# Optimization experiments

Measured on AMD Instinct MI355X. Metric: run time of the kernel, lower is better.

Reference implementation:

```python
import jax, jax.numpy as jnp
import numpy as np

N_START = 2
N_SUBUNITS = 1_000_000


def setup_inputs() -> dict:
    key = jax.random.key(0)
    k1, k2 = jax.random.split(key)
    # TMV-like helical parameters (Angstroms / degrees)
    rise = jnp.asarray(1.408, dtype=jnp.float32)
    twist = jnp.asarray(22.03, dtype=jnp.float32)
    initial_displacement = jax.random.normal(k1, (3,), dtype=jnp.float32) * 10.0
    # proper random rotation matrix for the first subunit via QR
    A = jax.random.normal(k2, (3, 3), dtype=jnp.float32)
    Q, _ = jnp.linalg.qr(A)
    initial_rotation = Q.astype(jnp.float32)
    return {
        "rise": rise,
        "twist": twist,
        "initial_displacement": initial_displacement,
        "initial_rotation": initial_rotation,
        "n_start": N_START,
        "n_subunits": N_SUBUNITS,
    }


def _helix_lattice(rise, twist_rad, r0, T0, n_start, n_subunits):
    """Closed-form rewrite of the affine lax.scan recurrences.

    Original position recurrence: r_{k+1} = R @ r_k + rise*ez with
    R = [[c, s, 0], [-s, c, 0], [0, 0, 1]] = Mz(-twist), so
    r_k = Mz(-k*twist) @ r0 + k*rise*ez (ez is invariant under Mz).
    Original rotation recurrence: T_k = (R^T)^k @ T0 = Mz(k*twist) @ T0.
    Symmetry rotation R_n = Mz(-sym_angle); Mz matrices commute/add angles.
    """
    dtype = r0.dtype
    k = jnp.arange(n_subunits, dtype=dtype)                                # (S,)
    sym = 2.0 * jnp.pi * jnp.arange(n_start, dtype=dtype) / n_start       # (H,)

    # ---- positions: Mz(-(sym + k*twist)) @ r0 + (k*rise - rise*S/2)*ez ----
    a = -(sym[:, None] + k[None, :] * twist_rad)                          # (H, S)
    ca, sa = jnp.cos(a), jnp.sin(a)
    x0, y0, z0 = r0[0], r0[1], r0[2]
    px = ca * x0 - sa * y0
    py = sa * x0 + ca * y0
    pz = jnp.broadcast_to(z0 + k * rise - rise * n_subunits / 2, a.shape)
    positions = jnp.stack([px, py, pz], axis=-1).reshape(n_start * n_subunits, 3)

    # ---- rotations: Mz(k*twist - sym) @ T0 ----
    b = k[None, :] * twist_rad - sym[:, None]                             # (H, S)
    cb, sb = jnp.cos(b), jnp.sin(b)
    zeros = jnp.zeros_like(cb)
    ones = jnp.ones_like(cb)
    M = jnp.stack(
        [
            jnp.stack([cb, -sb, zeros], axis=-1),
            jnp.stack([sb, cb, zeros], axis=-1),
            jnp.stack([zeros, zeros, ones], axis=-1),
        ],
        axis=-2,
    )                                                                      # (H, S, 3, 3)
    rotations = jnp.einsum("hsij,jk->hsik", M, T0).reshape(
        n_start * n_subunits, 3, 3
    )
    return positions, rotations


def reference(rise, twist, initial_displacement, initial_rotation, n_start, n_subunits):
    twist_rad = jnp.deg2rad(twist)  # degrees=True in the original module
    return _helix_lattice(
        rise, twist_rad, initial_displacement, initial_rotation, n_start, n_subunits
    )
```

## Files before the change

kernel.cpp:

```cpp
#include <hip/hip_runtime.h>
#include <math.h>

static constexpr int S_SUB   = 1000000;
static constexpr int H_START = 2;
static constexpr int CHK     = 128;
static constexpr int NCH_H   = (S_SUB + CHK - 1) / CHK;
static constexpr int NCH     = NCH_H * H_START;
static constexpr int TPB     = 256;
static constexpr int WPB     = TPB / 64;
static constexpr int NBLK    = 977;
static constexpr int NWAVE   = NBLK * WPB;

__global__ __launch_bounds__(256) void helix_kernel(
    const float* __restrict__ rise_p, const float* __restrict__ twist_p,
    const float* __restrict__ disp, const float* __restrict__ rot0,
    float* __restrict__ out )
{
    __shared__ alignas(16) float lds[WPB][CHK * 12];

    const int w = threadIdx.x >> 6;
    const int l = threadIdx.x & 63;
    float* __restrict__ PB = lds[w];
    float* __restrict__ RB = lds[w] + CHK * 3;

    const double t_rev  = (double)twist_p[0] * (1.0 / 360.0);
    const float  rise_f = rise_p[0];
    const float  zoff_f = (float)((double)disp[2]
                                  - (double)rise_p[0] * (double)S_SUB * 0.5);
    const float  x0 = disp[0], y0 = disp[1];
    const float  T00 = rot0[0], T01 = rot0[1], T02 = rot0[2];
    const float  T10 = rot0[3], T11 = rot0[4], T12 = rot0[5];
    const float  T20 = rot0[6], T21 = rot0[7], T22 = rot0[8];

    const int wave0 = blockIdx.x * WPB + w;
    for (int wid = wave0; wid < NCH; wid += NWAVE) {
        const int   h     = (wid >= NCH_H) ? 1 : 0;
        const int   c     = wid - h * NCH_H;
        const int   kbase = c * CHK;
        const int   nsub  = min(CHK, S_SUB - kbase);
        const float sgn   = h ? -1.0f : 1.0f;

#pragma unroll
        for (int j = 0; j < 2; ++j) {
            if (j * 64 < nsub) {
                const int    i   = l + 64 * j;
                const int    k   = kbase + i;
                const double trd = (double)k * t_rev;
                const float  fr  = (float)(trd - floor(trd));
                const float  c0  = sgn * __builtin_amdgcn_cosf(fr);
                const float  s0  = sgn * __builtin_amdgcn_sinf(fr);
                PB[i * 3 + 0] = c0 * x0 + s0 * y0;
                PB[i * 3 + 1] = c0 * y0 - s0 * x0;
                PB[i * 3 + 2] = (float)k * rise_f + zoff_f;
                RB[i * 9 + 0] = c0 * T00 - s0 * T10;
                RB[i * 9 + 1] = c0 * T01 - s0 * T11;
                RB[i * 9 + 2] = c0 * T02 - s0 * T12;
                RB[i * 9 + 3] = s0 * T00 + c0 * T10;
                RB[i * 9 + 4] = s0 * T01 + c0 * T11;
                RB[i * 9 + 5] = s0 * T02 + c0 * T12;
                RB[i * 9 + 6] = T20;
                RB[i * 9 + 7] = T21;
                RB[i * 9 + 8] = T22;
            }
        }

        const size_t hs = (size_t)h * S_SUB + (size_t)kbase;

        float2* __restrict__ pg = reinterpret_cast<float2*>(out + hs * 3);
        const int nf2p = (nsub * 3) >> 1;
#pragma unroll
        for (int i2 = 0; i2 < 3; ++i2) {
            const int m = l + 64 * i2;
            if (m < nf2p)
                pg[m] = *reinterpret_cast<const float2*>(&PB[2 * m]);
        }

        float2* __restrict__ rg = reinterpret_cast<float2*>(
            out + (size_t)3 * H_START * S_SUB + hs * 9);
        const int nf2r = (nsub * 9) >> 1;
#pragma unroll
        for (int i2 = 0; i2 < 9; ++i2) {
            const int m = l + 64 * i2;
            if (m < nf2r)
                rg[m] = *reinterpret_cast<const float2*>(&RB[2 * m]);
        }
    }
}

extern "C" void kernel_launch(void* const* d_in, const int* in_sizes, int n_in,
                              void* d_out, int out_size, void* d_ws, size_t ws_size,
                              hipStream_t stream) {
    const float* rise  = (const float*)d_in[0];
    const float* twist = (const float*)d_in[1];
    const float* disp  = (const float*)d_in[2];
    const float* rot0  = (const float*)d_in[3];
    float* out = (float*)d_out;

    helix_kernel<<<dim3(NBLK), TPB, 0, stream>>>(rise, twist, disp, rot0, out);
}
```

Before: 21.42 us.

## Drop LDS staging and compute each output float4 directly per thread

Replaces the per-wave LDS staging with float2 copies by a grid-stride loop in which each thread produces one float4 of the flat output. For its four elements the thread recomputes sine and cosine for up to two subunits and selects the value by index arithmetic. This removes LDS traffic and barriers and widens stores to 16 bytes. In exchange the trig and double-precision fraction work is repeated for every float4 rather than once per subunit, and the integer divides and selects add ALU work.

```diff
diff --git a/kernel.cpp b/kernel.cpp
--- a/kernel.cpp
+++ b/kernel.cpp
@@ -3,26 +3,22 @@
 
 static constexpr int S_SUB   = 1000000;
 static constexpr int H_START = 2;
-static constexpr int CHK     = 128;
-static constexpr int NCH_H   = (S_SUB + CHK - 1) / CHK;
-static constexpr int NCH     = NCH_H * H_START;
+static constexpr int POS_E   = 3 * H_START * S_SUB;
+static constexpr int TOT_E   = 12 * H_START * S_SUB;
+static constexpr int NQ      = TOT_E / 4;
 static constexpr int TPB     = 256;
-static constexpr int WPB     = TPB / 64;
-static constexpr int NBLK    = 977;
-static constexpr int NWAVE   = NBLK * WPB;
+static constexpr int NBLK    = 2048;
+static constexpr int NTHR    = NBLK * TPB;
+
+__device__ __forceinline__ float sel3(int x, float a, float b, float c) {
+    return x == 0 ? a : (x == 1 ? b : c);
+}
 
 __global__ __launch_bounds__(256) void helix_kernel(
     const float* __restrict__ rise_p, const float* __restrict__ twist_p,
     const float* __restrict__ disp, const float* __restrict__ rot0,
     float* __restrict__ out )
 {
-    __shared__ alignas(16) float lds[WPB][CHK * 12];
-
-    const int w = threadIdx.x >> 6;
-    const int l = threadIdx.x & 63;
-    float* __restrict__ PB = lds[w];
-    float* __restrict__ RB = lds[w] + CHK * 3;
-
     const double t_rev  = (double)twist_p[0] * (1.0 / 360.0);
     const float  rise_f = rise_p[0];
     const float  zoff_f = (float)((double)disp[2]
@@ -32,58 +28,80 @@
     const float  T10 = rot0[3], T11 = rot0[4], T12 = rot0[5];
     const float  T20 = rot0[6], T21 = rot0[7], T22 = rot0[8];
 
-    const int wave0 = blockIdx.x * WPB + w;
-    for (int wid = wave0; wid < NCH; wid += NWAVE) {
-        const int   h     = (wid >= NCH_H) ? 1 : 0;
-        const int   c     = wid - h * NCH_H;
-        const int   kbase = c * CHK;
-        const int   nsub  = min(CHK, S_SUB - kbase);
-        const float sgn   = h ? -1.0f : 1.0f;
+    float4* __restrict__ o4 = reinterpret_cast<float4*>(out);
+
+    for (int q = blockIdx.x * TPB + threadIdx.x; q < NQ; q += NTHR) {
+        const int e = q * 4;
+        float v0, v1, v2, v3;
+
+        if (e < POS_E) {
+            const int h  = (e >= 3 * S_SUB) ? 1 : 0;
+            const int e2 = e - h * 3 * S_SUB;
+            const int k0 = e2 / 3;
+            const int m0 = e2 - k0 * 3;
+            const float sgn = h ? -1.0f : 1.0f;
+
+            const double trd  = (double)k0 * t_rev;
+            const double trdB = trd + t_rev;
+            const float  frA  = (float)(trd  - floor(trd));
+            const float  frB  = (float)(trdB - floor(trdB));
+            const float cA = sgn * __builtin_amdgcn_cosf(frA);
+            const float sA = sgn * __builtin_amdgcn_sinf(frA);
+            const float cB = sgn * __builtin_amdgcn_cosf(frB);
+            const float sB = sgn * __builtin_amdgcn_sinf(frB);
+            const float pzA = (float)k0 * rise_f + zoff_f;
+            const float pzB = pzA + rise_f;
 
 #pragma unroll
-        for (int j = 0; j < 2; ++j) {
-            if (j * 64 < nsub) {
-                const int    i   = l + 64 * j;
-                const int    k   = kbase + i;
-                const double trd = (double)k * t_rev;
-                const float  fr  = (float)(trd - floor(trd));
-                const float  c0  = sgn * __builtin_amdgcn_cosf(fr);
-                const float  s0  = sgn * __builtin_amdgcn_sinf(fr);
-                PB[i * 3 + 0] = c0 * x0 + s0 * y0;
-                PB[i * 3 + 1] = c0 * y0 - s0 * x0;
-                PB[i * 3 + 2] = (float)k * rise_f + zoff_f;
-                RB[i * 9 + 0] = c0 * T00 - s0 * T10;
-                RB[i * 9 + 1] = c0 * T01 - s0 * T11;
-                RB[i * 9 + 2] = c0 * T02 - s0 * T12;
-                RB[i * 9 + 3] = s0 * T00 + c0 * T10;
-                RB[i * 9 + 4] = s0 * T01 + c0 * T11;
-                RB[i * 9 + 5] = s0 * T02 + c0 * T12;
-                RB[i * 9 + 6] = T20;
-                RB[i * 9 + 7] = T21;
-                RB[i * 9 + 8] = T22;
+            for (int j = 0; j < 4; ++j) {
+                const int  mj = m0 + j;
+                const bool hi = mj >= 3;
+                const int  cc = hi ? mj - 3 : mj;
+                const float c  = hi ? cB : cA;
+                const float s  = hi ? sB : sA;
+                const float pz = hi ? pzB : pzA;
+                const float val = sel3(cc, c * x0 + s * y0, c * y0 - s * x0, pz);
+                if (j == 0) v0 = val; else if (j == 1) v1 = val;
+                else if (j == 2) v2 = val; else v3 = val;
+            }
+        } else {
+            const int f  = e - POS_E;
+            const int h  = (f >= 9 * S_SUB) ? 1 : 0;
+            const int f2 = f - h * 9 * S_SUB;
+            const int k0 = f2 / 9;
+            const int m0 = f2 - k0 * 9;
+            const float sgn = h ? -1.0f : 1.0f;
+
+            const double trd  = (double)k0 * t_rev;
+            const double trdB = trd + t_rev;
+            const float  frA  = (float)(trd  - floor(trd));
+            const float  frB  = (float)(trdB - floor(trdB));
+            const float cA = sgn * __builtin_amdgcn_cosf(frA);
+            const float sA = sgn * __builtin_amdgcn_sinf(frA);
+            const float cB = sgn * __builtin_amdgcn_cosf(frB);
+            const float sB = sgn * __builtin_amdgcn_sinf(frB);
+
+#pragma unroll
+            for (int j = 0; j < 4; ++j) {
+                int mj = m0 + j;
+                const bool hi = mj >= 9;
+                mj = hi ? mj - 9 : mj;
+                const float c = hi ? cB : cA;
+                const float s = hi ? sB : sA;
+                const int g = (mj < 3) ? 0 : ((mj < 6) ? 1 : 2);
+                const int x = mj - 3 * g;
+                const float ta = sel3(x, T00, T01, T02);
+                const float tb = sel3(x, T10, T11, T12);
+                const float tc = sel3(x, T20, T21, T22);
+                const float pa = (g == 0) ? c : s;
+                const float pb = (g == 0) ? -s : c;
+                const float val = (g == 2) ? tc : (pa * ta + pb * tb);
+                if (j == 0) v0 = val; else if (j == 1) v1 = val;
+                else if (j == 2) v2 = val; else v3 = val;
             }
         }
 
-        const size_t hs = (size_t)h * S_SUB + (size_t)kbase;
-
-        float2* __restrict__ pg = reinterpret_cast<float2*>(out + hs * 3);
-        const int nf2p = (nsub * 3) >> 1;
-#pragma unroll
-        for (int i2 = 0; i2 < 3; ++i2) {
-            const int m = l + 64 * i2;
-            if (m < nf2p)
-                pg[m] = *reinterpret_cast<const float2*>(&PB[2 * m]);
-        }
-
-        float2* __restrict__ rg = reinterpret_cast<float2*>(
-            out + (size_t)3 * H_START * S_SUB + hs * 9);
-        const int nf2r = (nsub * 9) >> 1;
-#pragma unroll
-        for (int i2 = 0; i2 < 9; ++i2) {
-            const int m = l + 64 * i2;
-            if (m < nf2r)
-                rg[m] = *reinterpret_cast<const float2*>(&RB[2 * m]);
-        }
+        o4[q] = make_float4(v0, v1, v2, v3);
     }
 }
 
```

New measurement: 30.31 us. 1.41x slower.
